# Performance work log

Measured on AMD Instinct MI355X. Metric: run time of the kernel, lower is better.

Reference implementation:

```python
import jax, jax.numpy as jnp
import numpy as np

N_NODES = 100000
N_EDGES = 640000
D = 128
N_LAYERS = 4
N_GRAPHS = 512


def setup_inputs() -> dict:
    key = jax.random.key(0)
    ks = jax.random.split(key, 12)
    x = jax.random.normal(ks[0], (N_NODES, D), dtype=jnp.float32)
    edge_index = jax.random.randint(ks[1], (2, N_EDGES), 0, N_NODES, dtype=jnp.int64)
    batch = jnp.sort(jax.random.randint(ks[2], (N_NODES,), 0, N_GRAPHS, dtype=jnp.int64))
    s = 1.0 / np.sqrt(D)
    convW = jax.random.uniform(ks[3], (N_LAYERS, D, D), jnp.float32, -s, s)
    convB = jax.random.uniform(ks[4], (N_LAYERS, D), jnp.float32, -s, s)
    W1 = jax.random.uniform(ks[5], (D, D), jnp.float32, -s, s)
    b1 = jax.random.uniform(ks[6], (D,), jnp.float32, -s, s)
    W2 = jax.random.uniform(ks[7], (D, D), jnp.float32, -s, s)
    b2 = jax.random.uniform(ks[8], (D,), jnp.float32, -s, s)
    W3 = jax.random.uniform(ks[9], (D, 1), jnp.float32, -s, s)
    b3 = jax.random.uniform(ks[10], (1,), jnp.float32, -s, s)
    return {"x": x, "edge_index": edge_index, "batch": batch,
            "convW": convW, "convB": convB,
            "W1": W1, "b1": b1, "W2": W2, "b2": b2, "W3": W3, "b3": b3}


def reference(x, edge_index, batch, convW, convB, W1, b1, W2, b2, W3, b3):
    N = x.shape[0]
    # GCNConv default: add self-loops, symmetric deg^-1/2 normalization
    loops = jnp.arange(N, dtype=edge_index.dtype)
    src = jnp.concatenate([edge_index[0], loops])  # [E+N]
    dst = jnp.concatenate([edge_index[1], loops])
    deg = jax.ops.segment_sum(jnp.ones_like(dst, dtype=x.dtype), dst, num_segments=N)
    dinv = jnp.where(deg > 0, jax.lax.rsqrt(deg), 0.0)
    norm = (dinv[src] * dinv[dst])[:, None]  # [E+N, 1]
    h = x
    for i in range(N_LAYERS):
        hw = h @ convW[i]                                   # [N, D]
        msg = hw[src] * norm                                # gather + scale [E+N, D]
        agg = jax.ops.segment_sum(msg, dst, num_segments=N)  # scatter-add [N, D]
        h = jax.nn.relu(agg + convB[i])
    pooled = jax.ops.segment_sum(h, batch, num_segments=N_GRAPHS)  # [G, D]
    z = jax.nn.relu(pooled @ W1 + b1)
    z = jax.nn.relu(z @ W2 + b2)
    return jax.nn.sigmoid(z @ W3 + b3)  # [G, 1]
```

## Files before the change

kernel.cpp:

```cpp
#include <hip/hip_runtime.h>
#include <math.h>

#define D 128
#define LSTRIDE 136

typedef _Float16 half8 __attribute__((ext_vector_type(8)));
typedef _Float16 half4v __attribute__((ext_vector_type(4)));
typedef _Float16 half2v __attribute__((ext_vector_type(2)));
typedef float f32x4 __attribute__((ext_vector_type(4)));


__global__ void k_count(const int* __restrict__ ei, int* __restrict__ counts, int E) {
    int e0 = (blockIdx.x * blockDim.x + threadIdx.x) * 4;
    if (e0 + 3 < E) {
        int4 d4 = *(const int4*)(ei + E + e0);
        atomicAdd(&counts[d4.x], 1);
        atomicAdd(&counts[d4.y], 1);
        atomicAdd(&counts[d4.z], 1);
        atomicAdd(&counts[d4.w], 1);
    } else {
        for (int e = e0; e < E; e++) atomicAdd(&counts[ei[E + e]], 1);
    }
}

__global__ __launch_bounds__(256) void k_scan1(const int* __restrict__ counts,
                                               int* __restrict__ rowptr,
                                               int* __restrict__ bsums,
                                               float* __restrict__ dinv, int N) {
    __shared__ int sh[256];
    const int t = threadIdx.x;
    const int base = blockIdx.x * 1024 + t * 4;
    int c[4];
#pragma unroll
    for (int j = 0; j < 4; j++) c[j] = (base + j < N) ? counts[base + j] : 0;
#pragma unroll
    for (int j = 0; j < 4; j++)
        if (base + j < N) dinv[base + j] = rsqrtf((float)(c[j] + 1));
    int tsum = c[0] + c[1] + c[2] + c[3];
    sh[t] = tsum;
    __syncthreads();
    for (int off = 1; off < 256; off <<= 1) {
        int v = (t >= off) ? sh[t - off] : 0;
        __syncthreads();
        sh[t] += v;
        __syncthreads();
    }
    int run = (t == 0) ? 0 : sh[t - 1];
    if (t == 255) bsums[blockIdx.x] = sh[255];
#pragma unroll
    for (int j = 0; j < 4; j++) {
        if (base + j <= N) rowptr[base + j] = run;
        run += c[j];
    }
}

__global__ __launch_bounds__(128) void k_scan2(int* __restrict__ bsums, int NB) {
    __shared__ int sh[128];
    const int t = threadIdx.x;
    sh[t] = (t < NB) ? bsums[t] : 0;
    __syncthreads();
    for (int off = 1; off < 128; off <<= 1) {
        int v = (t >= off) ? sh[t - off] : 0;
        __syncthreads();
        sh[t] += v;
        __syncthreads();
    }
    if (t < NB) bsums[t] = (t == 0) ? 0 : sh[t - 1];
}

__global__ void k_scan3(int* __restrict__ rowptr, int* __restrict__ cursor,
                        const int* __restrict__ bsums, int N) {
    int i = blockIdx.x * blockDim.x + threadIdx.x;
    if (i <= N) {
        int v = rowptr[i] + bsums[i >> 10];
        rowptr[i] = v;
        if (i < N) cursor[i] = v;
    }
}

__global__ void k_fill(const int* __restrict__ ei, int* __restrict__ cursor,
                       int* __restrict__ srcs, int E) {
    int e0 = (blockIdx.x * blockDim.x + threadIdx.x) * 4;
    if (e0 + 3 < E) {
        int4 s4 = *(const int4*)(ei + e0);
        int4 d4 = *(const int4*)(ei + E + e0);
        int p0 = atomicAdd(&cursor[d4.x], 1);
        int p1 = atomicAdd(&cursor[d4.y], 1);
        int p2 = atomicAdd(&cursor[d4.z], 1);
        int p3 = atomicAdd(&cursor[d4.w], 1);
        srcs[p0] = s4.x;
        srcs[p1] = s4.y;
        srcs[p2] = s4.z;
        srcs[p3] = s4.w;
    } else {
        for (int e = e0; e < E; e++) {
            int pos = atomicAdd(&cursor[ei[E + e]], 1);
            srcs[pos] = ei[e];
        }
    }
}


__global__ void k_cvt(const float* __restrict__ x, const float* __restrict__ dinv,
                      _Float16* __restrict__ y, int n8) {
    int i = blockIdx.x * blockDim.x + threadIdx.x;
    if (i >= n8) return;
    float s = dinv[i >> 4];
    const float4 v0 = *(const float4*)(x + (size_t)i * 8);
    const float4 v1 = *(const float4*)(x + (size_t)i * 8 + 4);
    half8 h;
    h[0] = (_Float16)(v0.x * s); h[1] = (_Float16)(v0.y * s);
    h[2] = (_Float16)(v0.z * s); h[3] = (_Float16)(v0.w * s);
    h[4] = (_Float16)(v1.x * s); h[5] = (_Float16)(v1.y * s);
    h[6] = (_Float16)(v1.z * s); h[7] = (_Float16)(v1.w * s);
    *(half8*)(y + (size_t)i * 8) = h;
}


__global__ __launch_bounds__(256) void k_prepw(const float* __restrict__ convW,
                                               _Float16* __restrict__ Wf) {
    const int l = blockIdx.x >> 3;
    const int slot = (blockIdx.x & 7) * 256 + threadIdx.x;
    const float* W = convW + (size_t)l * D * D;
    const int p = slot >> 6, ln = slot & 63;
    const int s = p >> 3, c = p & 7;
    const int kbase = s * 32 + ((ln >> 4) << 3);
    const int n = (c << 4) + (ln & 15);
    half8 hv;
#pragma unroll
    for (int j = 0; j < 8; j++) hv[j] = (_Float16)W[(size_t)(kbase + j) * D + n];
    *(half8*)(Wf + (size_t)l * D * D + (size_t)slot * 8) = hv;
}


__global__ __launch_bounds__(512) void k_layer(
        const _Float16* __restrict__ gin,
        const int* __restrict__ rowptr, const int* __restrict__ srcs,
        const float* __restrict__ dinv,
        const _Float16* __restrict__ Wf,
        const float* __restrict__ bias,
        _Float16* __restrict__ gout, int N, int last) {
    __shared__ _Float16 S[128 * LSTRIDE];

    const int tid  = threadIdx.x;
    const int w    = tid >> 6;
    const int lane = tid & 63;
    const int q    = lane >> 4;
    const int l16  = lane & 15;
    const int nb0  = blockIdx.x * 128;

    const int cb = l16 * 8;
    for (int it = 0; it < 4; ++it) {
        const int nl = w * 16 + q * 4 + it;
        const int node = nb0 + nl;
        float a[8];
#pragma unroll
        for (int j = 0; j < 8; j++) a[j] = 0.f;

        if (node < N) {
            half8 sv = *(const half8*)(gin + (size_t)node * D + cb);
#pragma unroll
            for (int j = 0; j < 8; j++) a[j] = (float)sv[j];
            const int beg = rowptr[node];
            const int end = rowptr[node + 1];
            int e = beg;
            for (; e + 3 < end; e += 4) {
                int s0 = srcs[e], s1 = srcs[e + 1], s2 = srcs[e + 2], s3 = srcs[e + 3];
                half8 v0 = *(const half8*)(gin + (size_t)s0 * D + cb);
                half8 v1 = *(const half8*)(gin + (size_t)s1 * D + cb);
                half8 v2 = *(const half8*)(gin + (size_t)s2 * D + cb);
                half8 v3 = *(const half8*)(gin + (size_t)s3 * D + cb);
#pragma unroll
                for (int j = 0; j < 8; j++)
                    a[j] += ((float)v0[j] + (float)v1[j]) + ((float)v2[j] + (float)v3[j]);
            }
            for (; e < end; e++) {
                int s0 = srcs[e];
                half8 v0 = *(const half8*)(gin + (size_t)s0 * D + cb);
#pragma unroll
                for (int j = 0; j < 8; j++) a[j] += (float)v0[j];
            }
        }
        const float sc = (node < N) ? dinv[node] : 0.f;
        half8 o;
#pragma unroll
        for (int j = 0; j < 8; j++) o[j] = (_Float16)(a[j] * sc);
        *(half8*)(&S[nl * LSTRIDE + cb]) = o;
    }
    __syncthreads();

    f32x4 acc[8];
#pragma unroll
    for (int cc = 0; cc < 8; cc++) acc[cc] = (f32x4){0.f, 0.f, 0.f, 0.f};

    const int nl = w * 16 + l16;
#pragma unroll
    for (int s = 0; s < 4; s++) {
        half8 bf = *(const half8*)(&S[nl * LSTRIDE + s * 32 + q * 8]);
#pragma unroll
        for (int cc = 0; cc < 8; cc++) {
            half8 wh = *(const half8*)(Wf + (size_t)((s * 8 + cc) * 64 + lane) * 8);
            acc[cc] = __builtin_amdgcn_mfma_f32_16x16x32_f16(wh, bf, acc[cc], 0, 0, 0);
        }
    }

    const int node = nb0 + nl;
    if (node < N) {
        const float scale = last ? 1.0f : dinv[node];
        _Float16* rp = gout + (size_t)node * D + q * 4;
#pragma unroll
        for (int cc = 0; cc < 8; cc++) {
            const float4 bc = *(const float4*)(bias + cc * 16 + q * 4);
            half4v o;
            o[0] = (_Float16)(fmaxf(acc[cc][0] + bc.x, 0.f) * scale);
            o[1] = (_Float16)(fmaxf(acc[cc][1] + bc.y, 0.f) * scale);
            o[2] = (_Float16)(fmaxf(acc[cc][2] + bc.z, 0.f) * scale);
            o[3] = (_Float16)(fmaxf(acc[cc][3] + bc.w, 0.f) * scale);
            *(half4v*)(rp + cc * 16) = o;
        }
    }
}


__global__ __launch_bounds__(256) void k_poolhead(
        const _Float16* __restrict__ h, const int* __restrict__ batch,
        const float* __restrict__ W1, const float* __restrict__ b1,
        const float* __restrict__ W2, const float* __restrict__ b2,
        const float* __restrict__ W3, const float* __restrict__ b3,
        float* __restrict__ out, int N) {
    __shared__ int sb[2];
    __shared__ float part[4][D];
    __shared__ float v[D];
    __shared__ float z[D];
    __shared__ float red[D];

    const int g = blockIdx.x;
    const int t = threadIdx.x;

    if (t < 2) {
        int target = g + t;
        int lo = 0, hi = N;
        while (lo < hi) {
            int mid = (lo + hi) >> 1;
            if (batch[mid] < target) lo = mid + 1; else hi = mid;
        }
        sb[t] = lo;
    }
    __syncthreads();
    const int rs = sb[0], re = sb[1];

    const int w = t >> 6;
    const int lane = t & 63;
    const int c = lane * 2;

    float ax = 0.f, ay = 0.f;
    for (int r = rs + w; r < re; r += 4) {
        half2v vv = *(const half2v*)(h + (size_t)r * D + c);
        ax += (float)vv[0]; ay += (float)vv[1];
    }
    part[w][c] = ax;
    part[w][c + 1] = ay;
    __syncthreads();

    if (t < D) v[t] = part[0][t] + part[1][t] + part[2][t] + part[3][t];
    __syncthreads();

    if (t < D) {
        float s = b1[t];
        for (int k = 0; k < D; k++) s = fmaf(v[k], W1[(size_t)k * D + t], s);
        z[t] = fmaxf(s, 0.f);
    }
    __syncthreads();

    if (t < D) {
        float s = b2[t];
        for (int k = 0; k < D; k++) s = fmaf(z[k], W2[(size_t)k * D + t], s);
        red[t] = fmaxf(s, 0.f) * W3[t];
    }
    __syncthreads();
    for (int off = 64; off >= 1; off >>= 1) {
        if (t < off) red[t] += red[t + off];
        __syncthreads();
    }
    if (t == 0) out[g] = 1.f / (1.f + expf(-(red[0] + b3[0])));
}


extern "C" void kernel_launch(void* const* d_in, const int* in_sizes, int n_in,
                              void* d_out, int out_size, void* d_ws, size_t ws_size,
                              hipStream_t stream) {
    const float* x     = (const float*)d_in[0];
    const int*   ei    = (const int*)d_in[1];
    const int*   batch = (const int*)d_in[2];
    const float* convW = (const float*)d_in[3];
    const float* convB = (const float*)d_in[4];
    const float* W1 = (const float*)d_in[5];
    const float* b1 = (const float*)d_in[6];
    const float* W2 = (const float*)d_in[7];
    const float* b2 = (const float*)d_in[8];
    const float* W3 = (const float*)d_in[9];
    const float* b3 = (const float*)d_in[10];
    float* out = (float*)d_out;

    const int N = in_sizes[0] / D;
    const int E = in_sizes[1] / 2;
    const int G = out_size;
    const int NB = (N + 1023) / 1024;

    char* w = (char*)d_ws;
    size_t off = 0;
    auto alloc = [&](size_t bytes) -> char* {
        char* p = w + off;
        off += (bytes + 255) & ~(size_t)255;
        return p;
    };
    float*     dinv   = (float*)alloc((size_t)N * 4);
    _Float16*  gA     = (_Float16*)alloc((size_t)N * D * 2);
    _Float16*  gB     = (_Float16*)alloc((size_t)N * D * 2);
    _Float16*  Wf     = (_Float16*)alloc((size_t)4 * D * D * 2);
    int*       counts = (int*)alloc((size_t)N * 4);
    int*       rowptr = (int*)alloc((size_t)(N + 1) * 4);
    int*       cursor = (int*)alloc((size_t)N * 4);
    int*       srcs   = (int*)alloc((size_t)E * 4);
    int*       bsums  = (int*)alloc((size_t)NB * 4);

    hipMemsetAsync(counts, 0, (size_t)N * 4, stream);
    k_count<<<(E / 4 + 255) / 256, 256, 0, stream>>>(ei, counts, E);
    k_prepw<<<32, 256, 0, stream>>>(convW, Wf);
    k_scan1<<<NB, 256, 0, stream>>>(counts, rowptr, bsums, dinv, N);
    k_cvt<<<(N * D / 8 + 255) / 256, 256, 0, stream>>>(x, dinv, gA, N * D / 8);
    k_scan2<<<1, 128, 0, stream>>>(bsums, NB);
    k_scan3<<<(N + 1 + 255) / 256, 256, 0, stream>>>(rowptr, cursor, bsums, N);
    k_fill<<<(E / 4 + 255) / 256, 256, 0, stream>>>(ei, cursor, srcs, E);

    const int layer_grid = (N + 127) / 128;
    const _Float16* gi = gA;
    _Float16* go = gB;
    for (int l = 0; l < 4; l++) {
        k_layer<<<layer_grid, 512, 0, stream>>>(gi, rowptr, srcs, dinv,
                                                Wf + (size_t)l * D * D,
                                                convB + (size_t)l * D,
                                                go, N, l == 3);
        const _Float16* tmp = go;
        go = (_Float16*)gi;
        gi = tmp;
    }

    k_poolhead<<<G, 256, 0, stream>>>(gi, batch, W1, b1, W2, b2, W3, b3, out, N);
}
```

Before: 384.1 us.

## Record per-edge slot in count pass and shrink layer blocks to 64 nodes

The counting kernel now stores each edge's atomic return value as its position within its destination row. The fill kernel then writes srcs at rowptr+pidx without a second round of atomics, and the cursor array and its init in scan3 are removed. Separately, the layer kernel is launched with 256 threads over 64 nodes per block instead of 512 threads over 128, halving shared memory per block and doubling the grid. The cost is an extra E-sized int buffer written and read, and the change relies on the layer kernel's indexing scaling correctly with fewer waves.

```diff
diff --git a/kernel.cpp b/kernel.cpp
--- a/kernel.cpp
+++ b/kernel.cpp
@@ -3,6 +3,7 @@
 
 #define D 128
 #define LSTRIDE 136
+#define NPB 64
 
 typedef _Float16 half8 __attribute__((ext_vector_type(8)));
 typedef _Float16 half4v __attribute__((ext_vector_type(4)));
@@ -10,16 +11,19 @@
 typedef float f32x4 __attribute__((ext_vector_type(4)));
 
 
-__global__ void k_count(const int* __restrict__ ei, int* __restrict__ counts, int E) {
+__global__ void k_count(const int* __restrict__ ei, int* __restrict__ counts,
+                        int* __restrict__ pidx, int E) {
     int e0 = (blockIdx.x * blockDim.x + threadIdx.x) * 4;
     if (e0 + 3 < E) {
         int4 d4 = *(const int4*)(ei + E + e0);
-        atomicAdd(&counts[d4.x], 1);
-        atomicAdd(&counts[d4.y], 1);
-        atomicAdd(&counts[d4.z], 1);
-        atomicAdd(&counts[d4.w], 1);
+        int4 p;
+        p.x = atomicAdd(&counts[d4.x], 1);
+        p.y = atomicAdd(&counts[d4.y], 1);
+        p.z = atomicAdd(&counts[d4.z], 1);
+        p.w = atomicAdd(&counts[d4.w], 1);
+        *(int4*)(pidx + e0) = p;
     } else {
-        for (int e = e0; e < E; e++) atomicAdd(&counts[ei[E + e]], 1);
+        for (int e = e0; e < E; e++) pidx[e] = atomicAdd(&counts[ei[E + e]], 1);
     }
 }
 
@@ -68,35 +72,26 @@
     if (t < NB) bsums[t] = (t == 0) ? 0 : sh[t - 1];
 }
 
-__global__ void k_scan3(int* __restrict__ rowptr, int* __restrict__ cursor,
-                        const int* __restrict__ bsums, int N) {
+__global__ void k_scan3(int* __restrict__ rowptr, const int* __restrict__ bsums, int N) {
     int i = blockIdx.x * blockDim.x + threadIdx.x;
-    if (i <= N) {
-        int v = rowptr[i] + bsums[i >> 10];
-        rowptr[i] = v;
-        if (i < N) cursor[i] = v;
-    }
-}
-
-__global__ void k_fill(const int* __restrict__ ei, int* __restrict__ cursor,
-                       int* __restrict__ srcs, int E) {
+    if (i <= N) rowptr[i] += bsums[i >> 10];
+}
+
+__global__ void k_fill(const int* __restrict__ ei, const int* __restrict__ rowptr,
+                       const int* __restrict__ pidx, int* __restrict__ srcs, int E) {
     int e0 = (blockIdx.x * blockDim.x + threadIdx.x) * 4;
     if (e0 + 3 < E) {
         int4 s4 = *(const int4*)(ei + e0);
         int4 d4 = *(const int4*)(ei + E + e0);
-        int p0 = atomicAdd(&cursor[d4.x], 1);
-        int p1 = atomicAdd(&cursor[d4.y], 1);
-        int p2 = atomicAdd(&cursor[d4.z], 1);
-        int p3 = atomicAdd(&cursor[d4.w], 1);
-        srcs[p0] = s4.x;
-        srcs[p1] = s4.y;
-        srcs[p2] = s4.z;
-        srcs[p3] = s4.w;
+        int4 p4 = *(const int4*)(pidx + e0);
+        int r0 = rowptr[d4.x], r1 = rowptr[d4.y], r2 = rowptr[d4.z], r3 = rowptr[d4.w];
+        srcs[r0 + p4.x] = s4.x;
+        srcs[r1 + p4.y] = s4.y;
+        srcs[r2 + p4.z] = s4.z;
+        srcs[r3 + p4.w] = s4.w;
     } else {
-        for (int e = e0; e < E; e++) {
-            int pos = atomicAdd(&cursor[ei[E + e]], 1);
-            srcs[pos] = ei[e];
-        }
+        for (int e = e0; e < E; e++)
+            srcs[rowptr[ei[E + e]] + pidx[e]] = ei[e];
     }
 }
 
@@ -133,21 +128,21 @@
 }
 
 
-__global__ __launch_bounds__(512) void k_layer(
+__global__ __launch_bounds__(256) void k_layer(
         const _Float16* __restrict__ gin,
         const int* __restrict__ rowptr, const int* __restrict__ srcs,
         const float* __restrict__ dinv,
         const _Float16* __restrict__ Wf,
         const float* __restrict__ bias,
         _Float16* __restrict__ gout, int N, int last) {
-    __shared__ _Float16 S[128 * LSTRIDE];
+    __shared__ _Float16 S[NPB * LSTRIDE];
 
     const int tid  = threadIdx.x;
     const int w    = tid >> 6;
     const int lane = tid & 63;
     const int q    = lane >> 4;
     const int l16  = lane & 15;
-    const int nb0  = blockIdx.x * 128;
+    const int nb0  = blockIdx.x * NPB;
 
     const int cb = l16 * 8;
     for (int it = 0; it < 4; ++it) {
@@ -320,24 +315,24 @@
     _Float16*  Wf     = (_Float16*)alloc((size_t)4 * D * D * 2);
     int*       counts = (int*)alloc((size_t)N * 4);
     int*       rowptr = (int*)alloc((size_t)(N + 1) * 4);
-    int*       cursor = (int*)alloc((size_t)N * 4);
+    int*       pidx   = (int*)alloc((size_t)E * 4);
     int*       srcs   = (int*)alloc((size_t)E * 4);
     int*       bsums  = (int*)alloc((size_t)NB * 4);
 
     hipMemsetAsync(counts, 0, (size_t)N * 4, stream);
-    k_count<<<(E / 4 + 255) / 256, 256, 0, stream>>>(ei, counts, E);
+    k_count<<<(E / 4 + 255) / 256, 256, 0, stream>>>(ei, counts, pidx, E);
     k_prepw<<<32, 256, 0, stream>>>(convW, Wf);
     k_scan1<<<NB, 256, 0, stream>>>(counts, rowptr, bsums, dinv, N);
     k_cvt<<<(N * D / 8 + 255) / 256, 256, 0, stream>>>(x, dinv, gA, N * D / 8);
     k_scan2<<<1, 128, 0, stream>>>(bsums, NB);
-    k_scan3<<<(N + 1 + 255) / 256, 256, 0, stream>>>(rowptr, cursor, bsums, N);
-    k_fill<<<(E / 4 + 255) / 256, 256, 0, stream>>>(ei, cursor, srcs, E);
-
-    const int layer_grid = (N + 127) / 128;
+    k_scan3<<<(N + 1 + 255) / 256, 256, 0, stream>>>(rowptr, bsums, N);
+    k_fill<<<(E / 4 + 255) / 256, 256, 0, stream>>>(ei, rowptr, pidx, srcs, E);
+
+    const int layer_grid = (N + NPB - 1) / NPB;
     const _Float16* gi = gA;
     _Float16* go = gB;
     for (int l = 0; l < 4; l++) {
-        k_layer<<<layer_grid, 512, 0, stream>>>(gi, rowptr, srcs, dinv,
+        k_layer<<<layer_grid, 256, 0, stream>>>(gi, rowptr, srcs, dinv,
                                                 Wf + (size_t)l * D * D,
                                                 convB + (size_t)l * D,
                                                 go, N, l == 3);
```

Result: no change. 388.7 us (+1.2%).
